# Kernel tuning notes

Hardware: AMD Instinct MI355X
Metric: run time of the kernel (lower is better)

## Reference

```python
import jax, jax.numpy as jnp
import numpy as np

N = 50000


def gcn_conv(x, W, b, src, dst, deg_inv_sqrt):
    # h = x @ W, then symmetric-normalized aggregation with self-loops
    h = x @ W  # [N, out]
    norm = deg_inv_sqrt[src] * deg_inv_sqrt[dst]  # [E]
    agg = jax.ops.segment_sum(h[src] * norm[:, None], dst, num_segments=N)
    # self-loop contribution: norm_ii = deg_inv_sqrt[i]^2
    agg = agg + h * (deg_inv_sqrt * deg_inv_sqrt)[:, None]
    return agg + b


def setup_inputs() -> dict:
    key = jax.random.key(0)
    ks = jax.random.split(key, 8)
    F_in, H, C = 128, 128, 64
    x = jax.random.normal(ks[0], (N, F_in), dtype=jnp.float32)
    edge_index = jax.random.randint(ks[1], (2, 800000), 0, N, dtype=jnp.int64)
    s = 1.0 / np.sqrt(F_in)
    W1 = jax.random.uniform(ks[2], (F_in, H), jnp.float32, -s, s)
    b1 = jnp.zeros((H,), jnp.float32)
    W2 = jax.random.uniform(ks[3], (H, H), jnp.float32, -s, s)
    b2 = jnp.zeros((H,), jnp.float32)
    W3 = jax.random.uniform(ks[4], (H, C), jnp.float32, -s, s)
    b3 = jnp.zeros((C,), jnp.float32)
    return {"x": x, "edge_index": edge_index, "W1": W1, "b1": b1,
            "W2": W2, "b2": b2, "W3": W3, "b3": b3}


def reference(x, edge_index, W1, b1, W2, b2, W3, b3):
    src, dst = edge_index[0], edge_index[1]
    # degree with self-loops (edge weight 1): deg[i] = in-degree + 1
    deg = jnp.zeros((N,), x.dtype).at[dst].add(1.0) + 1.0
    dinv = jax.lax.rsqrt(deg)
    h = gcn_conv(x, W1, b1, src, dst, dinv)
    h = jax.nn.relu(h)  # dropout p=0 / eval -> identity
    h = gcn_conv(h, W2, b2, src, dst, dinv)
    h = jax.nn.relu(h)
    h = gcn_conv(h, W3, b3, src, dst, dinv)
    return jax.nn.log_softmax(h, axis=-1)
```

## Files before the change

### kernel.cpp

```cpp
#include <hip/hip_runtime.h>
#include <math.h>

typedef short short8 __attribute__((ext_vector_type(8)));
typedef float floatx4 __attribute__((ext_vector_type(4)));

__device__ __forceinline__ float4 ld4(const float* p) { return *reinterpret_cast<const float4*>(p); }
__device__ __forceinline__ void st4(float* p, float4 v) { *reinterpret_cast<float4*>(p) = v; }

__device__ __forceinline__ float bf2f(unsigned int u) { return __uint_as_float(u << 16); }
__device__ __forceinline__ unsigned int f2bf1(float f) {
    unsigned int x = __float_as_uint(f);
    return (x + 0x7fffu + ((x >> 16) & 1u)) >> 16;
}
__device__ __forceinline__ unsigned int f2bf2(float lo, float hi) {
    return f2bf1(lo) | (f2bf1(hi) << 16);
}
__device__ __forceinline__ void unpack8(uint4 v, float* f) {
    f[0] = bf2f(v.x & 0xffffu); f[1] = bf2f(v.x >> 16);
    f[2] = bf2f(v.y & 0xffffu); f[3] = bf2f(v.y >> 16);
    f[4] = bf2f(v.z & 0xffffu); f[5] = bf2f(v.z >> 16);
    f[6] = bf2f(v.w & 0xffffu); f[7] = bf2f(v.w >> 16);
}

__global__ __launch_bounds__(256) void k_count_prep(const int* __restrict__ dst, int* __restrict__ deg,
                                                    int* __restrict__ rank, int E, int nbE,
                                                    const float* __restrict__ W1, const float* __restrict__ W2,
                                                    const float* __restrict__ W3, unsigned short* __restrict__ Wt1,
                                                    unsigned short* __restrict__ Wt2, unsigned short* __restrict__ Wt3) {
    if ((int)blockIdx.x < nbE) {
        int e = blockIdx.x * 256 + threadIdx.x;
        if (e < E) rank[e] = atomicAdd(&deg[dst[e]], 1);
    } else {
        int t = (blockIdx.x - nbE) * 256 + threadIdx.x;
        if (t < 16384) {
            int k = t & 127, n = t >> 7;
            Wt1[n * 128 + k] = (unsigned short)f2bf1(W1[(size_t)k * 128 + n]);
        } else if (t < 32768) {
            int u = t - 16384;
            int k = u & 127, n = u >> 7;
            Wt2[n * 128 + k] = (unsigned short)f2bf1(W2[(size_t)k * 128 + n]);
        } else if (t < 40960) {
            int u = t - 32768;
            int k = u & 127, n = u >> 7;
            Wt3[n * 128 + k] = (unsigned short)f2bf1(W3[(size_t)k * 64 + n]);
        }
    }
}

__global__ __launch_bounds__(256) void k_dinv_reduce(const int* __restrict__ deg, float* __restrict__ dinv,
                                                     int* __restrict__ bsum, int n, int nbN) {
    __shared__ int s[256];
    int t = threadIdx.x;
    if ((int)blockIdx.x < nbN) {
        int i = blockIdx.x * 256 + t;
        if (i < n) dinv[i] = 1.0f / sqrtf((float)deg[i] + 1.0f);
        return;
    }
    int b = (int)blockIdx.x - nbN;
    int i = b * 256 + t;
    s[t] = (i < n) ? deg[i] : 0;
    __syncthreads();
    for (int off = 128; off > 0; off >>= 1) {
        if (t < off) s[t] += s[t + off];
        __syncthreads();
    }
    if (t == 0) bsum[b] = s[0];
}

__global__ __launch_bounds__(256) void k_scansmall_gemm1(const int* __restrict__ bsum, int* __restrict__ boff, int nb,
                                                         const float* __restrict__ X, const unsigned short* __restrict__ Wt,
                                                         const float* __restrict__ dinv,
                                                         unsigned short* __restrict__ O, int nrows) {
    constexpr int LDR = 136;
    __shared__ __align__(16) unsigned char smem[(64 * LDR + 128 * LDR) * 2];

    const int tid = threadIdx.x;
    if (blockIdx.x == 0) {
        int* s = (int*)smem;
        int v = (tid < nb) ? bsum[tid] : 0;
        s[tid] = v;
        __syncthreads();
        for (int off = 1; off < 256; off <<= 1) {
            int x = (tid >= off) ? s[tid - off] : 0;
            __syncthreads();
            s[tid] += x;
            __syncthreads();
        }
        if (tid < nb) boff[tid] = s[tid] - v;
        return;
    }

    unsigned short* sX = (unsigned short*)smem;
    unsigned short* sB = sX + 64 * LDR;
    const int row0 = ((int)blockIdx.x - 1) * 64;

#pragma unroll
    for (int i = 0; i < 4; ++i) {
        int idx = tid + i * 256;
        int r = idx >> 4, c8 = idx & 15;
        int grow = row0 + r;
        uint4 v = make_uint4(0, 0, 0, 0);
        if (grow < nrows) {
            float4 a = ld4(X + (size_t)grow * 128 + c8 * 8);
            float4 b = ld4(X + (size_t)grow * 128 + c8 * 8 + 4);
            v = make_uint4(f2bf2(a.x, a.y), f2bf2(a.z, a.w), f2bf2(b.x, b.y), f2bf2(b.z, b.w));
        }
        *reinterpret_cast<uint4*>(&sX[r * LDR + c8 * 8]) = v;
    }
#pragma unroll
    for (int i = 0; i < 8; ++i) {
        int idx = tid + i * 256;
        int nn = idx >> 4, c8 = idx & 15;
        *reinterpret_cast<uint4*>(&sB[nn * LDR + c8 * 8]) =
            *reinterpret_cast<const uint4*>(Wt + (size_t)nn * 128 + c8 * 8);
    }
    __syncthreads();

    const int lane = tid & 63;
    const int wave = tid >> 6;
    const int l15  = lane & 15;
    const int quad = lane >> 4;

    floatx4 acc[8];
#pragma unroll
    for (int j = 0; j < 8; ++j) acc[j] = (floatx4){0.f, 0.f, 0.f, 0.f};

    const unsigned short* xbase = &sX[(wave * 16 + l15) * LDR + quad * 8];
#pragma unroll
    for (int kk = 0; kk < 4; ++kk) {
        short8 xb = *reinterpret_cast<const short8*>(xbase + kk * 32);
#pragma unroll
        for (int j = 0; j < 8; ++j) {
            short8 wa = *reinterpret_cast<const short8*>(&sB[(j * 16 + l15) * LDR + quad * 8 + kk * 32]);
            acc[j] = __builtin_amdgcn_mfma_f32_16x16x32_bf16(wa, xb, acc[j], 0, 0, 0);
        }
    }

    int xrow = row0 + wave * 16 + l15;
    if (xrow < nrows) {
        float di = dinv[xrow];
#pragma unroll
        for (int j = 0; j < 8; ++j) {
            uint2 o = make_uint2(f2bf2(acc[j][0] * di, acc[j][1] * di), f2bf2(acc[j][2] * di, acc[j][3] * di));
            *reinterpret_cast<uint2*>(O + (size_t)xrow * 128 + j * 16 + quad * 4) = o;
        }
    }
}

__global__ __launch_bounds__(256) void k_scan_final(const int* __restrict__ deg, const int* __restrict__ boff,
                                                    int* __restrict__ row_off, int n) {
    __shared__ int s[256];
    int t = threadIdx.x;
    int i = blockIdx.x * 256 + t;
    int v = (i < n) ? deg[i] : 0;
    s[t] = v;
    __syncthreads();
    for (int off = 1; off < 256; off <<= 1) {
        int x = (t >= off) ? s[t - off] : 0;
        __syncthreads();
        s[t] += x;
        __syncthreads();
    }
    int incl = s[t] + boff[blockIdx.x];
    if (i < n) {
        row_off[i] = incl - v;
        if (i == n - 1) row_off[n] = incl;
    }
}

__global__ __launch_bounds__(256) void k_fill(const int* __restrict__ src, const int* __restrict__ dst,
                                              const int* __restrict__ rank, const int* __restrict__ roff,
                                              int* __restrict__ csrc, int E) {
    int e = blockIdx.x * 256 + threadIdx.x;
    if (e < E) csrc[roff[dst[e]] + rank[e]] = src[e];
}

template <int NC>
__global__ __launch_bounds__(256) void k_gemm_mfma(const unsigned short* __restrict__ X,
                                                   const unsigned short* __restrict__ Wt,
                                                   const float* __restrict__ dinv,
                                                   unsigned short* __restrict__ O, int nrows) {
    constexpr int LDR = 136;
    __shared__ unsigned short sX[64 * LDR];
    __shared__ unsigned short sB[NC * LDR];

    const int tid  = threadIdx.x;
    const int row0 = blockIdx.x * 64;

#pragma unroll
    for (int i = 0; i < 4; ++i) {
        int idx = tid + i * 256;
        int r = idx >> 4, c8 = idx & 15;
        int grow = row0 + r;
        uint4 v = make_uint4(0, 0, 0, 0);
        if (grow < nrows) v = *reinterpret_cast<const uint4*>(X + (size_t)grow * 128 + c8 * 8);
        *reinterpret_cast<uint4*>(&sX[r * LDR + c8 * 8]) = v;
    }
#pragma unroll
    for (int i = 0; i < NC / 16; ++i) {
        int idx = tid + i * 256;
        int n = idx >> 4, c8 = idx & 15;
        *reinterpret_cast<uint4*>(&sB[n * LDR + c8 * 8]) =
            *reinterpret_cast<const uint4*>(Wt + (size_t)n * 128 + c8 * 8);
    }
    __syncthreads();

    const int lane = tid & 63;
    const int wave = tid >> 6;
    const int l15  = lane & 15;
    const int quad = lane >> 4;

    floatx4 acc[NC / 16];
#pragma unroll
    for (int j = 0; j < NC / 16; ++j) acc[j] = (floatx4){0.f, 0.f, 0.f, 0.f};

    const unsigned short* xbase = &sX[(wave * 16 + l15) * LDR + quad * 8];
#pragma unroll
    for (int kk = 0; kk < 4; ++kk) {
        short8 xb = *reinterpret_cast<const short8*>(xbase + kk * 32);
#pragma unroll
        for (int j = 0; j < NC / 16; ++j) {
            short8 wa = *reinterpret_cast<const short8*>(&sB[(j * 16 + l15) * LDR + quad * 8 + kk * 32]);
            acc[j] = __builtin_amdgcn_mfma_f32_16x16x32_bf16(wa, xb, acc[j], 0, 0, 0);
        }
    }

    int xrow = row0 + wave * 16 + l15;
    if (xrow < nrows) {
        float di = dinv[xrow];
#pragma unroll
        for (int j = 0; j < NC / 16; ++j) {
            uint2 o = make_uint2(f2bf2(acc[j][0] * di, acc[j][1] * di), f2bf2(acc[j][2] * di, acc[j][3] * di));
            *reinterpret_cast<uint2*>(O + (size_t)xrow * NC + j * 16 + quad * 4) = o;
        }
    }
}

__global__ __launch_bounds__(256) void k_agg_relu(const unsigned short* __restrict__ H, const int* __restrict__ roff,
                                                  const int* __restrict__ csrc, const float* __restrict__ dinv,
                                                  const float* __restrict__ bias, unsigned short* __restrict__ O, int n) {
    int t    = blockIdx.x * 256 + threadIdx.x;
    int node = t >> 4;
    int f8   = (t & 15) * 8;
    if (node >= n) return;

    float a[8];
    {
        uint4 hv = *reinterpret_cast<const uint4*>(H + (size_t)node * 128 + f8);
        unpack8(hv, a);
    }

    int e  = roff[node];
    int e1 = roff[node + 1];
    for (; e + 3 < e1; e += 4) {
        int s[4];
        uint4 v[4];
#pragma unroll
        for (int u = 0; u < 4; ++u) s[u] = csrc[e + u];
#pragma unroll
        for (int u = 0; u < 4; ++u) v[u] = *reinterpret_cast<const uint4*>(H + (size_t)s[u] * 128 + f8);
#pragma unroll
        for (int u = 0; u < 4; ++u) {
            float g[8];
            unpack8(v[u], g);
#pragma unroll
            for (int i = 0; i < 8; ++i) a[i] += g[i];
        }
    }
    for (; e < e1; ++e) {
        uint4 v0 = *reinterpret_cast<const uint4*>(H + (size_t)csrc[e] * 128 + f8);
        float g0[8];
        unpack8(v0, g0);
#pragma unroll
        for (int i = 0; i < 8; ++i) a[i] += g0[i];
    }

    float di = dinv[node];
    float4 b0 = ld4(bias + f8);
    float4 b1 = ld4(bias + f8 + 4);
    float bb[8] = {b0.x, b0.y, b0.z, b0.w, b1.x, b1.y, b1.z, b1.w};
#pragma unroll
    for (int i = 0; i < 8; ++i) a[i] = fmaxf(a[i] * di + bb[i], 0.0f);

    uint4 ov = make_uint4(f2bf2(a[0], a[1]), f2bf2(a[2], a[3]), f2bf2(a[4], a[5]), f2bf2(a[6], a[7]));
    *reinterpret_cast<uint4*>(O + (size_t)node * 128 + f8) = ov;
}

__global__ __launch_bounds__(256) void k_agg_softmax(const unsigned short* __restrict__ H, const int* __restrict__ roff,
                                                     const int* __restrict__ csrc, const float* __restrict__ dinv,
                                                     const float* __restrict__ bias, float* __restrict__ O, int n) {
    int t    = blockIdx.x * 256 + threadIdx.x;
    int node = t >> 3;
    int f8   = (t & 7) * 8;
    if (node >= n) return;

    float a[8];
    {
        uint4 hv = *reinterpret_cast<const uint4*>(H + (size_t)node * 64 + f8);
        unpack8(hv, a);
    }

    int e  = roff[node];
    int e1 = roff[node + 1];
    for (; e + 7 < e1; e += 8) {
        int s[8];
        uint4 v[8];
#pragma unroll
        for (int u = 0; u < 8; ++u) s[u] = csrc[e + u];
#pragma unroll
        for (int u = 0; u < 8; ++u) v[u] = *reinterpret_cast<const uint4*>(H + (size_t)s[u] * 64 + f8);
#pragma unroll
        for (int u = 0; u < 8; ++u) {
            float gg[8];
            unpack8(v[u], gg);
#pragma unroll
            for (int i = 0; i < 8; ++i) a[i] += gg[i];
        }
    }
    if (e + 3 < e1) {
        int s[4];
        uint4 v[4];
#pragma unroll
        for (int u = 0; u < 4; ++u) s[u] = csrc[e + u];
#pragma unroll
        for (int u = 0; u < 4; ++u) v[u] = *reinterpret_cast<const uint4*>(H + (size_t)s[u] * 64 + f8);
#pragma unroll
        for (int u = 0; u < 4; ++u) {
            float gg[8];
            unpack8(v[u], gg);
#pragma unroll
            for (int i = 0; i < 8; ++i) a[i] += gg[i];
        }
        e += 4;
    }
    for (; e < e1; ++e) {
        uint4 v0 = *reinterpret_cast<const uint4*>(H + (size_t)csrc[e] * 64 + f8);
        float g0[8];
        unpack8(v0, g0);
#pragma unroll
        for (int i = 0; i < 8; ++i) a[i] += g0[i];
    }

    float di = dinv[node];
    float4 b0 = ld4(bias + f8);
    float4 b1 = ld4(bias + f8 + 4);
    float bb[8] = {b0.x, b0.y, b0.z, b0.w, b1.x, b1.y, b1.z, b1.w};
    float v[8];
#pragma unroll
    for (int i = 0; i < 8; ++i) v[i] = a[i] * di + bb[i];

    float m = v[0];
#pragma unroll
    for (int i = 1; i < 8; ++i) m = fmaxf(m, v[i]);
    m = fmaxf(m, __shfl_xor(m, 1));
    m = fmaxf(m, __shfl_xor(m, 2));
    m = fmaxf(m, __shfl_xor(m, 4));

    float ssum = 0.0f;
#pragma unroll
    for (int i = 0; i < 8; ++i) ssum += expf(v[i] - m);
    ssum += __shfl_xor(ssum, 1);
    ssum += __shfl_xor(ssum, 2);
    ssum += __shfl_xor(ssum, 4);
    float ls = logf(ssum);

    float* op = O + (size_t)node * 64 + f8;
    st4(op, make_float4(v[0] - m - ls, v[1] - m - ls, v[2] - m - ls, v[3] - m - ls));
    st4(op + 4, make_float4(v[4] - m - ls, v[5] - m - ls, v[6] - m - ls, v[7] - m - ls));
}

extern "C" void kernel_launch(void* const* d_in, const int* in_sizes, int n_in,
                              void* d_out, int out_size, void* d_ws, size_t ws_size,
                              hipStream_t stream) {
    const float* x  = (const float*)d_in[0];
    const int*   ei = (const int*)d_in[1];
    const float* W1 = (const float*)d_in[2];
    const float* b1 = (const float*)d_in[3];
    const float* W2 = (const float*)d_in[4];
    const float* b2 = (const float*)d_in[5];
    const float* W3 = (const float*)d_in[6];
    const float* b3 = (const float*)d_in[7];
    float* out = (float*)d_out;

    const int N = in_sizes[0] / 128;
    const int E = in_sizes[1] / 2;
    const int* src = ei;
    const int* dst = ei + E;

    char* ws = (char*)d_ws;
    size_t off = 0;
    auto alloc = [&](size_t bytes) -> char* {
        char* p = ws + off;
        off = (off + bytes + 255) & ~(size_t)255;
        return p;
    };
    int nb  = (N + 255) / 256;
    int nbE = (E + 255) / 256;
    int blocks64 = (N + 63) / 64;

    int*   deg     = (int*)alloc((size_t)N * 4);
    int*   row_off = (int*)alloc(((size_t)N + 1) * 4);
    float* dinv    = (float*)alloc((size_t)N * 4);
    int*   bsum    = (int*)alloc((size_t)nb * 4);
    int*   boff    = (int*)alloc((size_t)nb * 4);
    int*   rank    = (int*)alloc((size_t)E * 4);
    int*   csrc    = (int*)alloc((size_t)E * 4);
    unsigned short* Wt1  = (unsigned short*)alloc(128 * 128 * 2);
    unsigned short* Wt2  = (unsigned short*)alloc(128 * 128 * 2);
    unsigned short* Wt3  = (unsigned short*)alloc(64 * 128 * 2);
    unsigned short* bufA = (unsigned short*)alloc((size_t)N * 128 * 2);
    unsigned short* bufB = (unsigned short*)alloc((size_t)N * 128 * 2);
    unsigned short* bufC = (unsigned short*)alloc((size_t)N * 64 * 2);
    (void)ws_size; (void)n_in; (void)out_size;

    hipMemsetAsync(deg, 0, (size_t)N * 4, stream);
    k_count_prep<<<nbE + 160, 256, 0, stream>>>(dst, deg, rank, E, nbE, W1, W2, W3, Wt1, Wt2, Wt3);
    k_dinv_reduce<<<nb + nb, 256, 0, stream>>>(deg, dinv, bsum, N, nb);
    k_scansmall_gemm1<<<1 + blocks64, 256, 0, stream>>>(bsum, boff, nb, x, Wt1, dinv, bufA, N);
    k_scan_final<<<nb, 256, 0, stream>>>(deg, boff, row_off, N);
    k_fill<<<nbE, 256, 0, stream>>>(src, dst, rank, row_off, csrc, E);

    k_agg_relu<<<((size_t)N * 16 + 255) / 256, 256, 0, stream>>>(bufA, row_off, csrc, dinv, b1, bufB, N);
    k_gemm_mfma<128><<<blocks64, 256, 0, stream>>>(bufB, Wt2, dinv, bufA, N);
    k_agg_relu<<<((size_t)N * 16 + 255) / 256, 256, 0, stream>>>(bufA, row_off, csrc, dinv, b2, bufB, N);
    k_gemm_mfma<64><<<blocks64, 256, 0, stream>>>(bufB, Wt3, dinv, bufC, N);
    k_agg_softmax<<<((size_t)N * 8 + 255) / 256, 256, 0, stream>>>(bufC, row_off, csrc, dinv, b3, out, N);
}
```

Before: 251.5 us.

## Bucket nodes by in-degree and aggregate in degree-sorted order

Builds a degree histogram, scans it, and produces a permutation that groups nodes by in-degree (capped at 63). The aggregation kernels then process nodes in this permuted order so that threads in a wavefront get similar edge counts, which cuts divergence and load imbalance. The cost is extra histogram and scatter work in preprocessing, an extra indirection load per node, and less coalesced output writes and self-row reads, because adjacent threads now touch non-adjacent nodes.

```diff
diff --git a/kernel.cpp b/kernel.cpp
--- a/kernel.cpp
+++ b/kernel.cpp
@@ -48,12 +48,22 @@
 }
 
 __global__ __launch_bounds__(256) void k_dinv_reduce(const int* __restrict__ deg, float* __restrict__ dinv,
-                                                     int* __restrict__ bsum, int n, int nbN) {
+                                                     int* __restrict__ bsum, int* __restrict__ hist,
+                                                     int n, int nbN) {
     __shared__ int s[256];
+    __shared__ int lh[64];
     int t = threadIdx.x;
     if ((int)blockIdx.x < nbN) {
+        if (t < 64) lh[t] = 0;
+        __syncthreads();
         int i = blockIdx.x * 256 + t;
-        if (i < n) dinv[i] = 1.0f / sqrtf((float)deg[i] + 1.0f);
+        if (i < n) {
+            int d = deg[i];
+            dinv[i] = 1.0f / sqrtf((float)d + 1.0f);
+            atomicAdd(&lh[min(d, 63)], 1);
+        }
+        __syncthreads();
+        if (t < 64 && lh[t] != 0) atomicAdd(&hist[t], lh[t]);
         return;
     }
     int b = (int)blockIdx.x - nbN;
@@ -68,6 +78,7 @@
 }
 
 __global__ __launch_bounds__(256) void k_scansmall_gemm1(const int* __restrict__ bsum, int* __restrict__ boff, int nb,
+                                                         const int* __restrict__ hist, int* __restrict__ histcur,
                                                          const float* __restrict__ X, const unsigned short* __restrict__ Wt,
                                                          const float* __restrict__ dinv,
                                                          unsigned short* __restrict__ O, int nrows) {
@@ -89,10 +100,22 @@
         if (tid < nb) boff[tid] = s[tid] - v;
         return;
     }
+    if (blockIdx.x == 1) {
+        int* hsc = (int*)smem;
+        if (tid < 64) hsc[tid] = hist[tid];
+        __syncthreads();
+        if (tid == 0) {
+            int run = 0;
+            for (int c = 0; c < 64; ++c) { int v = hsc[c]; hsc[c] = run; run += v; }
+        }
+        __syncthreads();
+        if (tid < 64) histcur[tid] = hsc[tid];
+        return;
+    }
 
     unsigned short* sX = (unsigned short*)smem;
     unsigned short* sB = sX + 64 * LDR;
-    const int row0 = ((int)blockIdx.x - 1) * 64;
+    const int row0 = ((int)blockIdx.x - 2) * 64;
 
 #pragma unroll
     for (int i = 0; i < 4; ++i) {
@@ -148,24 +171,44 @@
 }
 
 __global__ __launch_bounds__(256) void k_scan_final(const int* __restrict__ deg, const int* __restrict__ boff,
-                                                    int* __restrict__ row_off, int n) {
+                                                    int* __restrict__ row_off, int* __restrict__ histcur,
+                                                    int* __restrict__ perm, int n, int nb) {
     __shared__ int s[256];
+    __shared__ int lh[64];
+    __shared__ int lbase[64];
     int t = threadIdx.x;
-    int i = blockIdx.x * 256 + t;
-    int v = (i < n) ? deg[i] : 0;
-    s[t] = v;
-    __syncthreads();
-    for (int off = 1; off < 256; off <<= 1) {
-        int x = (t >= off) ? s[t - off] : 0;
-        __syncthreads();
-        s[t] += x;
-        __syncthreads();
-    }
-    int incl = s[t] + boff[blockIdx.x];
-    if (i < n) {
-        row_off[i] = incl - v;
-        if (i == n - 1) row_off[n] = incl;
-    }
+    if ((int)blockIdx.x < nb) {
+        int i = blockIdx.x * 256 + t;
+        int v = (i < n) ? deg[i] : 0;
+        s[t] = v;
+        __syncthreads();
+        for (int off = 1; off < 256; off <<= 1) {
+            int x = (t >= off) ? s[t - off] : 0;
+            __syncthreads();
+            s[t] += x;
+            __syncthreads();
+        }
+        int incl = s[t] + boff[blockIdx.x];
+        if (i < n) {
+            row_off[i] = incl - v;
+            if (i == n - 1) row_off[n] = incl;
+        }
+        return;
+    }
+    int b = (int)blockIdx.x - nb;
+    int i = b * 256 + t;
+    if (t < 64) lh[t] = 0;
+    __syncthreads();
+    int c = 0, myr = 0;
+    bool valid = (i < n);
+    if (valid) {
+        c = min(deg[i], 63);
+        myr = atomicAdd(&lh[c], 1);
+    }
+    __syncthreads();
+    if (t < 64 && lh[t] != 0) lbase[t] = atomicAdd(&histcur[t], lh[t]);
+    __syncthreads();
+    if (valid) perm[lbase[c] + myr] = i;
 }
 
 __global__ __launch_bounds__(256) void k_fill(const int* __restrict__ src, const int* __restrict__ dst,
@@ -238,11 +281,13 @@
 
 __global__ __launch_bounds__(256) void k_agg_relu(const unsigned short* __restrict__ H, const int* __restrict__ roff,
                                                   const int* __restrict__ csrc, const float* __restrict__ dinv,
-                                                  const float* __restrict__ bias, unsigned short* __restrict__ O, int n) {
+                                                  const float* __restrict__ bias, const int* __restrict__ perm,
+                                                  unsigned short* __restrict__ O, int n) {
     int t    = blockIdx.x * 256 + threadIdx.x;
-    int node = t >> 4;
+    int g    = t >> 4;
     int f8   = (t & 15) * 8;
-    if (node >= n) return;
+    if (g >= n) return;
+    int node = perm[g];
 
     float a[8];
     {
@@ -261,10 +306,10 @@
         for (int u = 0; u < 4; ++u) v[u] = *reinterpret_cast<const uint4*>(H + (size_t)s[u] * 128 + f8);
 #pragma unroll
         for (int u = 0; u < 4; ++u) {
-            float g[8];
-            unpack8(v[u], g);
-#pragma unroll
-            for (int i = 0; i < 8; ++i) a[i] += g[i];
+            float g2[8];
+            unpack8(v[u], g2);
+#pragma unroll
+            for (int i = 0; i < 8; ++i) a[i] += g2[i];
         }
     }
     for (; e < e1; ++e) {
@@ -288,11 +333,13 @@
 
 __global__ __launch_bounds__(256) void k_agg_softmax(const unsigned short* __restrict__ H, const int* __restrict__ roff,
                                                      const int* __restrict__ csrc, const float* __restrict__ dinv,
-                                                     const float* __restrict__ bias, float* __restrict__ O, int n) {
+                                                     const float* __restrict__ bias, const int* __restrict__ perm,
+                                                     float* __restrict__ O, int n) {
     int t    = blockIdx.x * 256 + threadIdx.x;
-    int node = t >> 3;
+    int g    = t >> 3;
     int f8   = (t & 7) * 8;
-    if (node >= n) return;
+    if (g >= n) return;
+    int node = perm[g];
 
     float a[8];
     {
@@ -399,12 +446,15 @@
     int blocks64 = (N + 63) / 64;
 
     int*   deg     = (int*)alloc((size_t)N * 4);
+    int*   hist    = (int*)alloc(64 * 4);
+    int*   histcur = (int*)alloc(64 * 4);
     int*   row_off = (int*)alloc(((size_t)N + 1) * 4);
     float* dinv    = (float*)alloc((size_t)N * 4);
     int*   bsum    = (int*)alloc((size_t)nb * 4);
     int*   boff    = (int*)alloc((size_t)nb * 4);
     int*   rank    = (int*)alloc((size_t)E * 4);
     int*   csrc    = (int*)alloc((size_t)E * 4);
+    int*   perm    = (int*)alloc((size_t)N * 4);
     unsigned short* Wt1  = (unsigned short*)alloc(128 * 128 * 2);
     unsigned short* Wt2  = (unsigned short*)alloc(128 * 128 * 2);
     unsigned short* Wt3  = (unsigned short*)alloc(64 * 128 * 2);
@@ -413,16 +463,17 @@
     unsigned short* bufC = (unsigned short*)alloc((size_t)N * 64 * 2);
     (void)ws_size; (void)n_in; (void)out_size;
 
-    hipMemsetAsync(deg, 0, (size_t)N * 4, stream);
+    size_t degPad = (((size_t)N * 4 + 255) & ~(size_t)255);
+    hipMemsetAsync(deg, 0, degPad + 256, stream);
     k_count_prep<<<nbE + 160, 256, 0, stream>>>(dst, deg, rank, E, nbE, W1, W2, W3, Wt1, Wt2, Wt3);
-    k_dinv_reduce<<<nb + nb, 256, 0, stream>>>(deg, dinv, bsum, N, nb);
-    k_scansmall_gemm1<<<1 + blocks64, 256, 0, stream>>>(bsum, boff, nb, x, Wt1, dinv, bufA, N);
-    k_scan_final<<<nb, 256, 0, stream>>>(deg, boff, row_off, N);
+    k_dinv_reduce<<<nb + nb, 256, 0, stream>>>(deg, dinv, bsum, hist, N, nb);
+    k_scansmall_gemm1<<<2 + blocks64, 256, 0, stream>>>(bsum, boff, nb, hist, histcur, x, Wt1, dinv, bufA, N);
+    k_scan_final<<<nb + nb, 256, 0, stream>>>(deg, boff, row_off, histcur, perm, N, nb);
     k_fill<<<nbE, 256, 0, stream>>>(src, dst, rank, row_off, csrc, E);
 
-    k_agg_relu<<<((size_t)N * 16 + 255) / 256, 256, 0, stream>>>(bufA, row_off, csrc, dinv, b1, bufB, N);
+    k_agg_relu<<<((size_t)N * 16 + 255) / 256, 256, 0, stream>>>(bufA, row_off, csrc, dinv, b1, perm, bufB, N);
     k_gemm_mfma<128><<<blocks64, 256, 0, stream>>>(bufB, Wt2, dinv, bufA, N);
-    k_agg_relu<<<((size_t)N * 16 + 255) / 256, 256, 0, stream>>>(bufA, row_off, csrc, dinv, b2, bufB, N);
+    k_agg_relu<<<((size_t)N * 16 + 255) / 256, 256, 0, stream>>>(bufA, row_off, csrc, dinv, b2, perm, bufB, N);
     k_gemm_mfma<64><<<blocks64, 256, 0, stream>>>(bufB, Wt3, dinv, bufC, N);
-    k_agg_softmax<<<((size_t)N * 8 + 255) / 256, 256, 0, stream>>>(bufC, row_off, csrc, dinv, b3, out, N);
-}
+    k_agg_softmax<<<((size_t)N * 8 + 255) / 256, 256, 0, stream>>>(bufC, row_off, csrc, dinv, b3, perm, out, N);
+}
```

After: 253.6 us. No clear change (+0.8%).

## Split each node's edge list across two lane groups with masked 8-wide gathers

Applied to the files above, without the earlier changes.

The aggregation kernels now give each node twice as many threads. Each half of the group walks half of the node's neighbor list, and the two partial sums are combined with a cross-lane shuffle before the epilogue. The neighbor loop is rewritten as a fixed 8-wide batch with clamped indices and a 0/1 mask, replacing the remainder loops. This aims to raise memory-level parallelism and shorten per-thread gather chains for the average degree of about 16. The cost is twice the threads, redundant loads for masked tail lanes, and half the lanes sitting idle in the epilogue.

```diff
diff --git a/kernel.cpp b/kernel.cpp
--- a/kernel.cpp
+++ b/kernel.cpp
@@ -239,134 +239,138 @@
 __global__ __launch_bounds__(256) void k_agg_relu(const unsigned short* __restrict__ H, const int* __restrict__ roff,
                                                   const int* __restrict__ csrc, const float* __restrict__ dinv,
                                                   const float* __restrict__ bias, unsigned short* __restrict__ O, int n) {
-    int t    = blockIdx.x * 256 + threadIdx.x;
-    int node = t >> 4;
-    int f8   = (t & 15) * 8;
+    int t      = blockIdx.x * 256 + threadIdx.x;
+    int node   = t >> 5;
+    int lane32 = t & 31;
+    int half   = lane32 >> 4;
+    int f8     = (lane32 & 15) * 8;
     if (node >= n) return;
 
     float a[8];
-    {
+    if (half == 0) {
         uint4 hv = *reinterpret_cast<const uint4*>(H + (size_t)node * 128 + f8);
         unpack8(hv, a);
-    }
-
-    int e  = roff[node];
+    } else {
+#pragma unroll
+        for (int i = 0; i < 8; ++i) a[i] = 0.0f;
+    }
+
+    int e0 = roff[node];
     int e1 = roff[node + 1];
-    for (; e + 3 < e1; e += 4) {
-        int s[4];
-        uint4 v[4];
-#pragma unroll
-        for (int u = 0; u < 4; ++u) s[u] = csrc[e + u];
-#pragma unroll
-        for (int u = 0; u < 4; ++u) v[u] = *reinterpret_cast<const uint4*>(H + (size_t)s[u] * 128 + f8);
-#pragma unroll
-        for (int u = 0; u < 4; ++u) {
+    int mid = e0 + ((e1 - e0) >> 1);
+    int e  = half ? mid : e0;
+    int ee = half ? e1 : mid;
+
+    while (e < ee) {
+        int cnt = ee - e;
+        int idx[8];
+#pragma unroll
+        for (int u = 0; u < 8; ++u) idx[u] = csrc[e + min(u, cnt - 1)];
+        uint4 v[8];
+#pragma unroll
+        for (int u = 0; u < 8; ++u) v[u] = *reinterpret_cast<const uint4*>(H + (size_t)idx[u] * 128 + f8);
+#pragma unroll
+        for (int u = 0; u < 8; ++u) {
+            float mk = (u < cnt) ? 1.0f : 0.0f;
             float g[8];
             unpack8(v[u], g);
 #pragma unroll
-            for (int i = 0; i < 8; ++i) a[i] += g[i];
-        }
-    }
-    for (; e < e1; ++e) {
-        uint4 v0 = *reinterpret_cast<const uint4*>(H + (size_t)csrc[e] * 128 + f8);
-        float g0[8];
-        unpack8(v0, g0);
-#pragma unroll
-        for (int i = 0; i < 8; ++i) a[i] += g0[i];
-    }
-
-    float di = dinv[node];
-    float4 b0 = ld4(bias + f8);
-    float4 b1 = ld4(bias + f8 + 4);
-    float bb[8] = {b0.x, b0.y, b0.z, b0.w, b1.x, b1.y, b1.z, b1.w};
-#pragma unroll
-    for (int i = 0; i < 8; ++i) a[i] = fmaxf(a[i] * di + bb[i], 0.0f);
-
-    uint4 ov = make_uint4(f2bf2(a[0], a[1]), f2bf2(a[2], a[3]), f2bf2(a[4], a[5]), f2bf2(a[6], a[7]));
-    *reinterpret_cast<uint4*>(O + (size_t)node * 128 + f8) = ov;
+            for (int i = 0; i < 8; ++i) a[i] = fmaf(mk, g[i], a[i]);
+        }
+        e += 8;
+    }
+
+#pragma unroll
+    for (int i = 0; i < 8; ++i) a[i] += __shfl_xor(a[i], 16);
+
+    if (half == 0) {
+        float di = dinv[node];
+        float4 b0 = ld4(bias + f8);
+        float4 b1 = ld4(bias + f8 + 4);
+        float bb[8] = {b0.x, b0.y, b0.z, b0.w, b1.x, b1.y, b1.z, b1.w};
+#pragma unroll
+        for (int i = 0; i < 8; ++i) a[i] = fmaxf(a[i] * di + bb[i], 0.0f);
+
+        uint4 ov = make_uint4(f2bf2(a[0], a[1]), f2bf2(a[2], a[3]), f2bf2(a[4], a[5]), f2bf2(a[6], a[7]));
+        *reinterpret_cast<uint4*>(O + (size_t)node * 128 + f8) = ov;
+    }
 }
 
 __global__ __launch_bounds__(256) void k_agg_softmax(const unsigned short* __restrict__ H, const int* __restrict__ roff,
                                                      const int* __restrict__ csrc, const float* __restrict__ dinv,
                                                      const float* __restrict__ bias, float* __restrict__ O, int n) {
-    int t    = blockIdx.x * 256 + threadIdx.x;
-    int node = t >> 3;
-    int f8   = (t & 7) * 8;
+    int t      = blockIdx.x * 256 + threadIdx.x;
+    int node   = t >> 4;
+    int lane16 = t & 15;
+    int half   = lane16 >> 3;
+    int f8     = (lane16 & 7) * 8;
     if (node >= n) return;
 
     float a[8];
-    {
+    if (half == 0) {
         uint4 hv = *reinterpret_cast<const uint4*>(H + (size_t)node * 64 + f8);
         unpack8(hv, a);
-    }
-
-    int e  = roff[node];
+    } else {
+#pragma unroll
+        for (int i = 0; i < 8; ++i) a[i] = 0.0f;
+    }
+
+    int e0 = roff[node];
     int e1 = roff[node + 1];
-    for (; e + 7 < e1; e += 8) {
-        int s[8];
+    int mid = e0 + ((e1 - e0) >> 1);
+    int e  = half ? mid : e0;
+    int ee = half ? e1 : mid;
+
+    while (e < ee) {
+        int cnt = ee - e;
+        int idx[8];
+#pragma unroll
+        for (int u = 0; u < 8; ++u) idx[u] = csrc[e + min(u, cnt - 1)];
         uint4 v[8];
 #pragma unroll
-        for (int u = 0; u < 8; ++u) s[u] = csrc[e + u];
-#pragma unroll
-        for (int u = 0; u < 8; ++u) v[u] = *reinterpret_cast<const uint4*>(H + (size_t)s[u] * 64 + f8);
+        for (int u = 0; u < 8; ++u) v[u] = *reinterpret_cast<const uint4*>(H + (size_t)idx[u] * 64 + f8);
 #pragma unroll
         for (int u = 0; u < 8; ++u) {
-            float gg[8];
-            unpack8(v[u], gg);
-#pragma unroll
-            for (int i = 0; i < 8; ++i) a[i] += gg[i];
-        }
-    }
-    if (e + 3 < e1) {
-        int s[4];
-        uint4 v[4];
-#pragma unroll
-        for (int u = 0; u < 4; ++u) s[u] = csrc[e + u];
-#pragma unroll
-        for (int u = 0; u < 4; ++u) v[u] = *reinterpret_cast<const uint4*>(H + (size_t)s[u] * 64 + f8);
-#pragma unroll
-        for (int u = 0; u < 4; ++u) {
-            float gg[8];
-            unpack8(v[u], gg);
-#pragma unroll
-            for (int i = 0; i < 8; ++i) a[i] += gg[i];
-        }
-        e += 4;
-    }
-    for (; e < e1; ++e) {
-        uint4 v0 = *reinterpret_cast<const uint4*>(H + (size_t)csrc[e] * 64 + f8);
-        float g0[8];
-        unpack8(v0, g0);
-#pragma unroll
-        for (int i = 0; i < 8; ++i) a[i] += g0[i];
-    }
-
-    float di = dinv[node];
-    float4 b0 = ld4(bias + f8);
-    float4 b1 = ld4(bias + f8 + 4);
-    float bb[8] = {b0.x, b0.y, b0.z, b0.w, b1.x, b1.y, b1.z, b1.w};
-    float v[8];
-#pragma unroll
-    for (int i = 0; i < 8; ++i) v[i] = a[i] * di + bb[i];
-
-    float m = v[0];
-#pragma unroll
-    for (int i = 1; i < 8; ++i) m = fmaxf(m, v[i]);
-    m = fmaxf(m, __shfl_xor(m, 1));
-    m = fmaxf(m, __shfl_xor(m, 2));
-    m = fmaxf(m, __shfl_xor(m, 4));
-
-    float ssum = 0.0f;
-#pragma unroll
-    for (int i = 0; i < 8; ++i) ssum += expf(v[i] - m);
-    ssum += __shfl_xor(ssum, 1);
-    ssum += __shfl_xor(ssum, 2);
-    ssum += __shfl_xor(ssum, 4);
-    float ls = logf(ssum);
-
-    float* op = O + (size_t)node * 64 + f8;
-    st4(op, make_float4(v[0] - m - ls, v[1] - m - ls, v[2] - m - ls, v[3] - m - ls));
-    st4(op + 4, make_float4(v[4] - m - ls, v[5] - m - ls, v[6] - m - ls, v[7] - m - ls));
+            float mk = (u < cnt) ? 1.0f : 0.0f;
+            float g[8];
+            unpack8(v[u], g);
+#pragma unroll
+            for (int i = 0; i < 8; ++i) a[i] = fmaf(mk, g[i], a[i]);
+        }
+        e += 8;
+    }
+
+#pragma unroll
+    for (int i = 0; i < 8; ++i) a[i] += __shfl_xor(a[i], 8);
+
+    if (half == 0) {
+        float di = dinv[node];
+        float4 b0 = ld4(bias + f8);
+        float4 b1 = ld4(bias + f8 + 4);
+        float bb[8] = {b0.x, b0.y, b0.z, b0.w, b1.x, b1.y, b1.z, b1.w};
+        float v[8];
+#pragma unroll
+        for (int i = 0; i < 8; ++i) v[i] = a[i] * di + bb[i];
+
+        float m = v[0];
+#pragma unroll
+        for (int i = 1; i < 8; ++i) m = fmaxf(m, v[i]);
+        m = fmaxf(m, __shfl_xor(m, 1));
+        m = fmaxf(m, __shfl_xor(m, 2));
+        m = fmaxf(m, __shfl_xor(m, 4));
+
+        float ssum = 0.0f;
+#pragma unroll
+        for (int i = 0; i < 8; ++i) ssum += expf(v[i] - m);
+        ssum += __shfl_xor(ssum, 1);
+        ssum += __shfl_xor(ssum, 2);
+        ssum += __shfl_xor(ssum, 4);
+        float ls = logf(ssum);
+
+        float* op = O + (size_t)node * 64 + f8;
+        st4(op, make_float4(v[0] - m - ls, v[1] - m - ls, v[2] - m - ls, v[3] - m - ls));
+        st4(op + 4, make_float4(v[4] - m - ls, v[5] - m - ls, v[6] - m - ls, v[7] - m - ls));
+    }
 }
 
 extern "C" void kernel_launch(void* const* d_in, const int* in_sizes, int n_in,
@@ -420,9 +424,9 @@
     k_scan_final<<<nb, 256, 0, stream>>>(deg, boff, row_off, N);
     k_fill<<<nbE, 256, 0, stream>>>(src, dst, rank, row_off, csrc, E);
 
-    k_agg_relu<<<((size_t)N * 16 + 255) / 256, 256, 0, stream>>>(bufA, row_off, csrc, dinv, b1, bufB, N);
+    k_agg_relu<<<((size_t)N * 32 + 255) / 256, 256, 0, stream>>>(bufA, row_off, csrc, dinv, b1, bufB, N);
     k_gemm_mfma<128><<<blocks64, 256, 0, stream>>>(bufB, Wt2, dinv, bufA, N);
-    k_agg_relu<<<((size_t)N * 16 + 255) / 256, 256, 0, stream>>>(bufA, row_off, csrc, dinv, b2, bufB, N);
+    k_agg_relu<<<((size_t)N * 32 + 255) / 256, 256, 0, stream>>>(bufA, row_off, csrc, dinv, b2, bufB, N);
     k_gemm_mfma<64><<<blocks64, 256, 0, stream>>>(bufB, Wt3, dinv, bufC, N);
-    k_agg_softmax<<<((size_t)N * 8 + 255) / 256, 256, 0, stream>>>(bufC, row_off, csrc, dinv, b3, out, N);
-}
+    k_agg_softmax<<<((size_t)N * 16 + 255) / 256, 256, 0, stream>>>(bufC, row_off, csrc, dinv, b3, out, N);
+}
```

New measurement: 257.5 us. 2.4% more time.
